# Performance work log

Hardware: AMD Instinct MI355X
Metric: run time of the kernel (lower is better)

## Reference

```python
import jax, jax.numpy as jnp
import numpy as np

N = 100000   # nodes
E = 1600000  # edges (avg degree 16)
D = 32       # feature dim

def setup_inputs() -> dict:
    key = jax.random.key(0)
    k1, k2, k3, k4 = jax.random.split(key, 4)
    feat = jax.random.normal(k1, (N, D), dtype=jnp.float32)
    e_feat = jax.random.normal(k2, (E, 1), dtype=jnp.float32)
    src = jax.random.randint(k3, (E,), 0, N)
    dst = jax.random.randint(k4, (E,), 0, N)
    return {"feat": feat, "e_feat": e_feat, "src": src, "dst": dst}

def reference(feat, e_feat, src, dst):
    n = feat.shape[0]
    ones = jnp.ones(src.shape[0], dtype=feat.dtype)
    # degrees computed on the full graph (before self-loop removal), as in DGL code
    out_deg = jax.ops.segment_sum(ones, src, num_segments=n)
    in_deg = jax.ops.segment_sum(ones, dst, num_segments=n)
    src_norm = jnp.power(jnp.clip(out_deg, 1.0, None), -0.5)[:, None]  # [N,1]
    dst_norm = jnp.power(jnp.clip(in_deg, 1.0, None), -0.5)[:, None]   # [N,1]
    # remove_self_loop: mask out self-loop edges in the aggregation only
    mask = (src != dst).astype(feat.dtype)[:, None]                    # [E,1]
    # u_mul_e: gather normalized src features, multiply by edge weight
    msg = (feat * src_norm)[src] * (e_feat * mask)                     # [E,D]
    agg = jax.ops.segment_sum(msg, dst, num_segments=n)                # [N,D]
    out = feat - agg * dst_norm
    return jnp.sum(jnp.abs(out), axis=1)                               # [N]
```

## Files before the change

kernel.cpp:

```cpp
#include <hip/hip_runtime.h>

#define D 32
#define RANGE 128
#define RMAX 800
#define JC 512
#define CHUNKMAX 3200
#define CAP 2304
#define SJC 256
#define SCHUNKMAX 6400
#define STRIDE 2560
#define SSTRIDE 2560
#define CPAD 16

__device__ __forceinline__ int scan512(int x, int* wp, int t) {
    int lane = t & 63, w = t >> 6;
    #pragma unroll
    for (int d = 1; d < 64; d <<= 1) {
        int y = __shfl_up(x, d, 64);
        if (lane >= d) x += y;
    }
    if (lane == 63) wp[w] = x;
    __syncthreads();
    int off = 0;
    #pragma unroll
    for (int i = 0; i < 7; i++) if (i < w) off += wp[i];
    return x + off;
}

__global__ __launch_bounds__(256) void zero_cur(int* __restrict__ p, int m) {
    int i = blockIdx.x * 256 + threadIdx.x;
    if (i < m) p[i] = 0;
}

__global__ __launch_bounds__(512) void fused_sort(
        const int* __restrict__ src, const int* __restrict__ dst,
        const float* __restrict__ ef,
        uint2* __restrict__ recsR, unsigned* __restrict__ srcsR,
        int* __restrict__ gcurD, int* __restrict__ gcurS,
        int E, int R, int chunk, int chunkS) {
    __shared__ __align__(16) char arena[32000];
    __shared__ int wp[8];
    int t = threadIdx.x;
    int* cnt = (int*)(arena + 25600);
    int* cur = (int*)(arena + 28800);

    if (blockIdx.x < JC) {
        int j = blockIdx.x;
        uint2* sd = (uint2*)arena;
        int e0 = j * chunk, e1 = min(E, e0 + chunk);
        for (int i = t; i < RMAX; i += 512) cnt[i] = 0;
        __syncthreads();
        for (int e = e0 + 2 * t; e < e1; e += 1024) {
            if (e + 1 < e1) {
                int2 d2 = *(const int2*)(dst + e);
                atomicAdd(&cnt[d2.x >> 7], 1);
                atomicAdd(&cnt[d2.y >> 7], 1);
            } else {
                atomicAdd(&cnt[dst[e] >> 7], 1);
            }
        }
        __syncthreads();
        int v0 = cnt[t];
        int incl0 = scan512(v0, wp, t);
        int tot0 = wp[0] + wp[1] + wp[2] + wp[3] + wp[4] + wp[5] + wp[6] + wp[7];
        __syncthreads();
        int i1 = t + 512;
        int v1 = (i1 < RMAX) ? cnt[i1] : 0;
        int incl1 = scan512(v1, wp, t);
        cur[t] = incl0 - v0;
        if (i1 < RMAX) cur[i1] = tot0 + incl1 - v1;
        __syncthreads();
        for (int e = e0 + t; e < e1; e += 512) {
            int s = src[e], d = dst[e];
            float w = (s == d) ? 0.0f : ef[e];
            int pos = atomicAdd(&cur[d >> 7], 1);
            sd[pos] = make_uint2((unsigned)s | ((unsigned)(d & (RANGE - 1)) << 17),
                                 __float_as_uint(w));
        }
        __syncthreads();
        for (int i = t; i < R; i += 512) {
            int c = cnt[i];
            if (c) {
                int g = atomicAdd(&gcurD[i * CPAD], c);
                int ls = cur[i] - c;
                uint2* dp = recsR + (size_t)i * STRIDE + g;
                for (int k = 0; k < c; k++) dp[k] = sd[ls + k];
            }
        }
    } else {
        int j = blockIdx.x - JC;
        unsigned* ids = (unsigned*)arena;
        int e0 = j * chunkS, e1 = min(E, e0 + chunkS);
        for (int i = t; i < RMAX; i += 512) cnt[i] = 0;
        __syncthreads();
        for (int e = e0 + 2 * t; e < e1; e += 1024) {
            if (e + 1 < e1) {
                int2 s2 = *(const int2*)(src + e);
                atomicAdd(&cnt[s2.x >> 7], 1);
                atomicAdd(&cnt[s2.y >> 7], 1);
            } else {
                atomicAdd(&cnt[src[e] >> 7], 1);
            }
        }
        __syncthreads();
        int v0 = cnt[t];
        int incl0 = scan512(v0, wp, t);
        int tot0 = wp[0] + wp[1] + wp[2] + wp[3] + wp[4] + wp[5] + wp[6] + wp[7];
        __syncthreads();
        int i1 = t + 512;
        int v1 = (i1 < RMAX) ? cnt[i1] : 0;
        int incl1 = scan512(v1, wp, t);
        cur[t] = incl0 - v0;
        if (i1 < RMAX) cur[i1] = tot0 + incl1 - v1;
        __syncthreads();
        for (int e = e0 + t; e < e1; e += 512) {
            unsigned s = (unsigned)src[e];
            int pos = atomicAdd(&cur[s >> 7], 1);
            ids[pos] = s;
        }
        __syncthreads();
        for (int i = t; i < R; i += 512) {
            int c = cnt[i];
            if (c) {
                int g = atomicAdd(&gcurS[i * CPAD], c);
                int ls = cur[i] - c;
                unsigned* dp = srcsR + (size_t)i * SSTRIDE + g;
                for (int k = 0; k < c; k++) dp[k] = ids[ls + k];
            }
        }
    }
}

__device__ __forceinline__ unsigned short f2bf(float x) {
    unsigned u = __float_as_uint(x);
    u += 0x7FFFu + ((u >> 16) & 1u);
    return (unsigned short)(u >> 16);
}

__global__ __launch_bounds__(512) void srcnorm_convert(
        const unsigned* __restrict__ srcsR, const int* __restrict__ gcurS,
        const float* __restrict__ feat, unsigned short* __restrict__ featb,
        int n, int R) {
    __shared__ int cnt[RANGE];
    int r = blockIdx.x, t = threadIdx.x;
    int base = r * RANGE, lim = min(n - base, RANGE);
    if (t < RANGE) cnt[t] = 0;
    __syncthreads();
    int total = gcurS[r * CPAD];
    const unsigned* p = srcsR + (size_t)r * SSTRIDE;
    for (int i = t; i < total; i += 512)
        atomicAdd(&cnt[p[i] - (unsigned)base], 1);
    __syncthreads();
    int total4 = lim * 8;
    for (int i = t; i < total4; i += 512) {
        int row = i >> 3;
        float sn = rsqrtf((float)max(cnt[row], 1));
        float4 f = ((const float4*)(feat + (size_t)(base + row) * D))[i & 7];
        ushort4 u;
        u.x = f2bf(f.x * sn); u.y = f2bf(f.y * sn);
        u.z = f2bf(f.z * sn); u.w = f2bf(f.w * sn);
        ((ushort4*)(featb + (size_t)(base + row) * D))[i & 7] = u;
    }
}

__global__ __launch_bounds__(512) void gather_kernel(
        const float* __restrict__ feat, const unsigned short* __restrict__ featb,
        const uint2* __restrict__ recsR, const int* __restrict__ gcurD,
        float* __restrict__ out, int n, int R) {
    __shared__ uint2 raw[CAP];
    __shared__ uint2 srec[CAP];
    __shared__ int indeg[RANGE];
    __shared__ int pre[RANGE + 1];
    __shared__ int wp[8];
    int r = blockIdx.x, t = threadIdx.x;
    int base = r * RANGE, lim = min(n - base, RANGE);
    int total = gcurD[r * CPAD];
    bool ovf = total > CAP;
    const uint2* reg = recsR + (size_t)r * STRIDE;
    if (t < RANGE) indeg[t] = 0;
    __syncthreads();
    if (!ovf) {
        for (int i = t; i < total; i += 512) {
            uint2 rec = reg[i];
            raw[i] = rec;
            atomicAdd(&indeg[rec.x >> 17], 1);
        }
    } else {
        for (int i = t; i < total; i += 512)
            atomicAdd(&indeg[reg[i].x >> 17], 1);
    }
    __syncthreads();
    int vv = (t < RANGE) ? indeg[t] : 0;
    int incl2 = scan512(vv, wp, t);
    if (t < RANGE) pre[t + 1] = incl2;
    if (t == 0) pre[0] = 0;
    __syncthreads();
    if (t < RANGE) indeg[t] = pre[t];
    __syncthreads();
    if (!ovf) {
        for (int i = t; i < total; i += 512) {
            uint2 rec = raw[i];
            int dl = rec.x >> 17;
            int pos = atomicAdd(&indeg[dl], 1);
            srec[pos] = make_uint2(rec.x & 0x1FFFFu, rec.y);
        }
    }
    __syncthreads();
    int node = t >> 2;
    int cch = t & 3;
    if (node >= lim) return;
    int p0i = pre[node];
    int cnt = pre[node + 1] - p0i;
    float a0 = 0.f, a1 = 0.f, a2 = 0.f, a3 = 0.f, a4 = 0.f, a5 = 0.f, a6 = 0.f, a7 = 0.f;
    if (!ovf) {
        const uint2* sp = srec + p0i;
        int i = 0;
        for (; i + 4 <= cnt; i += 4) {
            uint2 q0 = sp[i], q1 = sp[i + 1], q2 = sp[i + 2], q3 = sp[i + 3];
            uint4 b0 = ((const uint4*)(featb + (size_t)q0.x * D))[cch];
            uint4 b1 = ((const uint4*)(featb + (size_t)q1.x * D))[cch];
            uint4 b2 = ((const uint4*)(featb + (size_t)q2.x * D))[cch];
            uint4 b3 = ((const uint4*)(featb + (size_t)q3.x * D))[cch];
            float w0 = __uint_as_float(q0.y), w1 = __uint_as_float(q1.y);
            float w2 = __uint_as_float(q2.y), w3 = __uint_as_float(q3.y);
            a0 += __uint_as_float(b0.x << 16) * w0 + __uint_as_float(b1.x << 16) * w1
                + __uint_as_float(b2.x << 16) * w2 + __uint_as_float(b3.x << 16) * w3;
            a1 += __uint_as_float(b0.x & 0xFFFF0000u) * w0 + __uint_as_float(b1.x & 0xFFFF0000u) * w1
                + __uint_as_float(b2.x & 0xFFFF0000u) * w2 + __uint_as_float(b3.x & 0xFFFF0000u) * w3;
            a2 += __uint_as_float(b0.y << 16) * w0 + __uint_as_float(b1.y << 16) * w1
                + __uint_as_float(b2.y << 16) * w2 + __uint_as_float(b3.y << 16) * w3;
            a3 += __uint_as_float(b0.y & 0xFFFF0000u) * w0 + __uint_as_float(b1.y & 0xFFFF0000u) * w1
                + __uint_as_float(b2.y & 0xFFFF0000u) * w2 + __uint_as_float(b3.y & 0xFFFF0000u) * w3;
            a4 += __uint_as_float(b0.z << 16) * w0 + __uint_as_float(b1.z << 16) * w1
                + __uint_as_float(b2.z << 16) * w2 + __uint_as_float(b3.z << 16) * w3;
            a5 += __uint_as_float(b0.z & 0xFFFF0000u) * w0 + __uint_as_float(b1.z & 0xFFFF0000u) * w1
                + __uint_as_float(b2.z & 0xFFFF0000u) * w2 + __uint_as_float(b3.z & 0xFFFF0000u) * w3;
            a6 += __uint_as_float(b0.w << 16) * w0 + __uint_as_float(b1.w << 16) * w1
                + __uint_as_float(b2.w << 16) * w2 + __uint_as_float(b3.w << 16) * w3;
            a7 += __uint_as_float(b0.w & 0xFFFF0000u) * w0 + __uint_as_float(b1.w & 0xFFFF0000u) * w1
                + __uint_as_float(b2.w & 0xFFFF0000u) * w2 + __uint_as_float(b3.w & 0xFFFF0000u) * w3;
        }
        for (; i < cnt; i++) {
            uint2 q = sp[i];
            uint4 b = ((const uint4*)(featb + (size_t)q.x * D))[cch];
            float w = __uint_as_float(q.y);
            a0 += __uint_as_float(b.x << 16) * w;
            a1 += __uint_as_float(b.x & 0xFFFF0000u) * w;
            a2 += __uint_as_float(b.y << 16) * w;
            a3 += __uint_as_float(b.y & 0xFFFF0000u) * w;
            a4 += __uint_as_float(b.z << 16) * w;
            a5 += __uint_as_float(b.z & 0xFFFF0000u) * w;
            a6 += __uint_as_float(b.w << 16) * w;
            a7 += __uint_as_float(b.w & 0xFFFF0000u) * w;
        }
    } else {
        for (int k = 0; k < total; k++) {
            uint2 rec = reg[k];
            if ((int)(rec.x >> 17) == node) {
                uint4 b = ((const uint4*)(featb + (size_t)(rec.x & 0x1FFFFu) * D))[cch];
                float w = __uint_as_float(rec.y);
                a0 += __uint_as_float(b.x << 16) * w;
                a1 += __uint_as_float(b.x & 0xFFFF0000u) * w;
                a2 += __uint_as_float(b.y << 16) * w;
                a3 += __uint_as_float(b.y & 0xFFFF0000u) * w;
                a4 += __uint_as_float(b.z << 16) * w;
                a5 += __uint_as_float(b.z & 0xFFFF0000u) * w;
                a6 += __uint_as_float(b.w << 16) * w;
                a7 += __uint_as_float(b.w & 0xFFFF0000u) * w;
            }
        }
    }
    float dn = rsqrtf((float)max(cnt, 1));
    const float4* fr = (const float4*)(feat + (size_t)(base + node) * D);
    float4 fA = fr[cch * 2];
    float4 fB = fr[cch * 2 + 1];
    float v = fabsf(fA.x - a0 * dn) + fabsf(fA.y - a1 * dn) +
              fabsf(fA.z - a2 * dn) + fabsf(fA.w - a3 * dn) +
              fabsf(fB.x - a4 * dn) + fabsf(fB.y - a5 * dn) +
              fabsf(fB.z - a6 * dn) + fabsf(fB.w - a7 * dn);
    v += __shfl_xor(v, 1, 4);
    v += __shfl_xor(v, 2, 4);
    if (cch == 0) out[base + node] = v;
}

extern "C" void kernel_launch(void* const* d_in, const int* in_sizes, int n_in,
                              void* d_out, int out_size, void* d_ws, size_t ws_size,
                              hipStream_t stream) {
    const float* feat   = (const float*)d_in[0];
    const float* e_feat = (const float*)d_in[1];
    const int*   src    = (const int*)d_in[2];
    const int*   dst    = (const int*)d_in[3];
    const int E = in_sizes[2];
    const int n = in_sizes[0] / D;
    float* out = (float*)d_out;

    const int R = (n + RANGE - 1) / RANGE;
    const int chunk  = (((E + JC  - 1) / JC ) + 1) & ~1;
    const int chunkS = (((E + SJC - 1) / SJC) + 1) & ~1;

    char* p = (char*)d_ws;
    uint2* recsR    = (uint2*)p;    p += ((size_t)R * STRIDE * 8 + 15) & ~(size_t)15;
    unsigned* srcsR = (unsigned*)p; p += ((size_t)R * SSTRIDE * 4 + 15) & ~(size_t)15;
    int* gcurD      = (int*)p;      p += ((size_t)R * CPAD * 4 + 15) & ~(size_t)15;
    int* gcurS      = (int*)p;      p += ((size_t)R * CPAD * 4 + 15) & ~(size_t)15;
    unsigned short* featb = (unsigned short*)p;

    const int mcur = R * CPAD * 2;
    zero_cur<<<(mcur + 255) / 256, 256, 0, stream>>>(gcurD, mcur);

    fused_sort<<<JC + SJC, 512, 0, stream>>>(src, dst, e_feat, recsR, srcsR,
                                             gcurD, gcurS, E, R, chunk, chunkS);

    srcnorm_convert<<<R, 512, 0, stream>>>(srcsR, gcurS, feat, featb, n, R);

    gather_kernel<<<R, 512, 0, stream>>>(feat, featb, recsR, gcurD, out, n, R);
}
```

Before: 146.0 us.

## Coalesce bucket scatter, shrink src ids to bytes, use fp32 normalized features

The sort kernel now stores a per-record range tag in shared memory and writes bucketed records back in one flat loop, so consecutive threads store consecutive records. Previously each thread copied a whole bucket serially. Chunk sizes are now fixed (5000 dst edges, 9000 src edges per block) with a larger shared arena, and source ids are stored as 8-bit local offsets, which cuts write and read traffic. The normalized feature table is kept in fp32 instead of bf16, which doubles gather bytes but removes conversion work and rounding error. The src-degree histogram is also split into two shared copies to reduce atomic contention.

```diff
diff --git a/kernel.cpp b/kernel.cpp
--- a/kernel.cpp
+++ b/kernel.cpp
@@ -3,14 +3,15 @@
 #define D 32
 #define RANGE 128
 #define RMAX 800
-#define JC 512
-#define CHUNKMAX 3200
 #define CAP 2304
-#define SJC 256
-#define SCHUNKMAX 6400
 #define STRIDE 2560
 #define SSTRIDE 2560
 #define CPAD 16
+#define DCH 5000
+#define SCH 9000
+#define CNT_OFF 50000
+#define CUR_OFF 53200
+#define ARENA_SZ 56400
 
 __device__ __forceinline__ int scan512(int x, int* wp, int t) {
     int lane = t & 63, w = t >> 6;
@@ -35,19 +36,20 @@
 __global__ __launch_bounds__(512) void fused_sort(
         const int* __restrict__ src, const int* __restrict__ dst,
         const float* __restrict__ ef,
-        uint2* __restrict__ recsR, unsigned* __restrict__ srcsR,
+        uint2* __restrict__ recsR, unsigned char* __restrict__ srcsR,
         int* __restrict__ gcurD, int* __restrict__ gcurS,
-        int E, int R, int chunk, int chunkS) {
-    __shared__ __align__(16) char arena[32000];
+        int E, int DJC) {
+    __shared__ __align__(16) char arena[ARENA_SZ];
     __shared__ int wp[8];
     int t = threadIdx.x;
-    int* cnt = (int*)(arena + 25600);
-    int* cur = (int*)(arena + 28800);
-
-    if (blockIdx.x < JC) {
+    int* cnt = (int*)(arena + CNT_OFF);
+    int* cur = (int*)(arena + CUR_OFF);
+
+    if ((int)blockIdx.x < DJC) {
         int j = blockIdx.x;
         uint2* sd = (uint2*)arena;
-        int e0 = j * chunk, e1 = min(E, e0 + chunk);
+        unsigned short* rg16 = (unsigned short*)(arena + 40000);
+        int e0 = j * DCH, e1 = min(E, e0 + DCH), cntE = e1 - e0;
         for (int i = t; i < RMAX; i += 512) cnt[i] = 0;
         __syncthreads();
         for (int e = e0 + 2 * t; e < e1; e += 1024) {
@@ -73,24 +75,30 @@
         for (int e = e0 + t; e < e1; e += 512) {
             int s = src[e], d = dst[e];
             float w = (s == d) ? 0.0f : ef[e];
-            int pos = atomicAdd(&cur[d >> 7], 1);
-            sd[pos] = make_uint2((unsigned)s | ((unsigned)(d & (RANGE - 1)) << 17),
+            int rg = d >> 7;
+            int pos = atomicAdd(&cur[rg], 1);
+            sd[pos] = make_uint2((unsigned)s | ((unsigned)(d & 127) << 17),
                                  __float_as_uint(w));
-        }
-        __syncthreads();
-        for (int i = t; i < R; i += 512) {
+            rg16[pos] = (unsigned short)rg;
+        }
+        __syncthreads();
+        for (int i = t; i < RMAX; i += 512) {
             int c = cnt[i];
             if (c) {
                 int g = atomicAdd(&gcurD[i * CPAD], c);
-                int ls = cur[i] - c;
-                uint2* dp = recsR + (size_t)i * STRIDE + g;
-                for (int k = 0; k < c; k++) dp[k] = sd[ls + k];
-            }
+                cnt[i] = g - (cur[i] - c);
+            }
+        }
+        __syncthreads();
+        for (int i = t; i < cntE; i += 512) {
+            int rg = rg16[i];
+            recsR[(size_t)rg * STRIDE + cnt[rg] + i] = sd[i];
         }
     } else {
-        int j = blockIdx.x - JC;
-        unsigned* ids = (unsigned*)arena;
-        int e0 = j * chunkS, e1 = min(E, e0 + chunkS);
+        int j = blockIdx.x - DJC;
+        unsigned char* sid = (unsigned char*)arena;
+        unsigned short* rg16 = (unsigned short*)(arena + 9000);
+        int e0 = j * SCH, e1 = min(E, e0 + SCH), cntE = e1 - e0;
         for (int i = t; i < RMAX; i += 512) cnt[i] = 0;
         __syncthreads();
         for (int e = e0 + 2 * t; e < e1; e += 1024) {
@@ -114,57 +122,59 @@
         if (i1 < RMAX) cur[i1] = tot0 + incl1 - v1;
         __syncthreads();
         for (int e = e0 + t; e < e1; e += 512) {
-            unsigned s = (unsigned)src[e];
-            int pos = atomicAdd(&cur[s >> 7], 1);
-            ids[pos] = s;
-        }
-        __syncthreads();
-        for (int i = t; i < R; i += 512) {
+            int s = src[e];
+            int rg = s >> 7;
+            int pos = atomicAdd(&cur[rg], 1);
+            sid[pos] = (unsigned char)(s & 127);
+            rg16[pos] = (unsigned short)rg;
+        }
+        __syncthreads();
+        for (int i = t; i < RMAX; i += 512) {
             int c = cnt[i];
             if (c) {
                 int g = atomicAdd(&gcurS[i * CPAD], c);
-                int ls = cur[i] - c;
-                unsigned* dp = srcsR + (size_t)i * SSTRIDE + g;
-                for (int k = 0; k < c; k++) dp[k] = ids[ls + k];
-            }
-        }
-    }
-}
-
-__device__ __forceinline__ unsigned short f2bf(float x) {
-    unsigned u = __float_as_uint(x);
-    u += 0x7FFFu + ((u >> 16) & 1u);
-    return (unsigned short)(u >> 16);
+                cnt[i] = g - (cur[i] - c);
+            }
+        }
+        __syncthreads();
+        for (int i = t; i < cntE; i += 512) {
+            int rg = rg16[i];
+            srcsR[(size_t)rg * SSTRIDE + cnt[rg] + i] = sid[i];
+        }
+    }
 }
 
 __global__ __launch_bounds__(512) void srcnorm_convert(
-        const unsigned* __restrict__ srcsR, const int* __restrict__ gcurS,
-        const float* __restrict__ feat, unsigned short* __restrict__ featb,
+        const unsigned char* __restrict__ srcsR, const int* __restrict__ gcurS,
+        const float* __restrict__ feat, float* __restrict__ featn,
         int n, int R) {
+    __shared__ int h[2][RANGE];
     __shared__ int cnt[RANGE];
     int r = blockIdx.x, t = threadIdx.x;
     int base = r * RANGE, lim = min(n - base, RANGE);
-    if (t < RANGE) cnt[t] = 0;
+    if (t < 256) h[t >> 7][t & 127] = 0;
     __syncthreads();
     int total = gcurS[r * CPAD];
-    const unsigned* p = srcsR + (size_t)r * SSTRIDE;
+    const unsigned char* p = srcsR + (size_t)r * SSTRIDE;
+    int cp = (t >> 8) & 1;
     for (int i = t; i < total; i += 512)
-        atomicAdd(&cnt[p[i] - (unsigned)base], 1);
+        atomicAdd(&h[cp][p[i]], 1);
+    __syncthreads();
+    if (t < RANGE) cnt[t] = h[0][t] + h[1][t];
     __syncthreads();
     int total4 = lim * 8;
     for (int i = t; i < total4; i += 512) {
         int row = i >> 3;
         float sn = rsqrtf((float)max(cnt[row], 1));
         float4 f = ((const float4*)(feat + (size_t)(base + row) * D))[i & 7];
-        ushort4 u;
-        u.x = f2bf(f.x * sn); u.y = f2bf(f.y * sn);
-        u.z = f2bf(f.z * sn); u.w = f2bf(f.w * sn);
-        ((ushort4*)(featb + (size_t)(base + row) * D))[i & 7] = u;
+        float4 o;
+        o.x = f.x * sn; o.y = f.y * sn; o.z = f.z * sn; o.w = f.w * sn;
+        ((float4*)(featn + (size_t)(base + row) * D))[i & 7] = o;
     }
 }
 
 __global__ __launch_bounds__(512) void gather_kernel(
-        const float* __restrict__ feat, const unsigned short* __restrict__ featb,
+        const float* __restrict__ feat, const float* __restrict__ featn,
         const uint2* __restrict__ recsR, const int* __restrict__ gcurD,
         float* __restrict__ out, int n, int R) {
     __shared__ uint2 raw[CAP];
@@ -217,56 +227,42 @@
         int i = 0;
         for (; i + 4 <= cnt; i += 4) {
             uint2 q0 = sp[i], q1 = sp[i + 1], q2 = sp[i + 2], q3 = sp[i + 3];
-            uint4 b0 = ((const uint4*)(featb + (size_t)q0.x * D))[cch];
-            uint4 b1 = ((const uint4*)(featb + (size_t)q1.x * D))[cch];
-            uint4 b2 = ((const uint4*)(featb + (size_t)q2.x * D))[cch];
-            uint4 b3 = ((const uint4*)(featb + (size_t)q3.x * D))[cch];
+            const float4* f0 = (const float4*)(featn + (size_t)q0.x * D) + cch * 2;
+            const float4* f1 = (const float4*)(featn + (size_t)q1.x * D) + cch * 2;
+            const float4* f2 = (const float4*)(featn + (size_t)q2.x * D) + cch * 2;
+            const float4* f3 = (const float4*)(featn + (size_t)q3.x * D) + cch * 2;
+            float4 A0 = f0[0], B0 = f0[1];
+            float4 A1 = f1[0], B1 = f1[1];
+            float4 A2 = f2[0], B2 = f2[1];
+            float4 A3 = f3[0], B3 = f3[1];
             float w0 = __uint_as_float(q0.y), w1 = __uint_as_float(q1.y);
             float w2 = __uint_as_float(q2.y), w3 = __uint_as_float(q3.y);
-            a0 += __uint_as_float(b0.x << 16) * w0 + __uint_as_float(b1.x << 16) * w1
-                + __uint_as_float(b2.x << 16) * w2 + __uint_as_float(b3.x << 16) * w3;
-            a1 += __uint_as_float(b0.x & 0xFFFF0000u) * w0 + __uint_as_float(b1.x & 0xFFFF0000u) * w1
-                + __uint_as_float(b2.x & 0xFFFF0000u) * w2 + __uint_as_float(b3.x & 0xFFFF0000u) * w3;
-            a2 += __uint_as_float(b0.y << 16) * w0 + __uint_as_float(b1.y << 16) * w1
-                + __uint_as_float(b2.y << 16) * w2 + __uint_as_float(b3.y << 16) * w3;
-            a3 += __uint_as_float(b0.y & 0xFFFF0000u) * w0 + __uint_as_float(b1.y & 0xFFFF0000u) * w1
-                + __uint_as_float(b2.y & 0xFFFF0000u) * w2 + __uint_as_float(b3.y & 0xFFFF0000u) * w3;
-            a4 += __uint_as_float(b0.z << 16) * w0 + __uint_as_float(b1.z << 16) * w1
-                + __uint_as_float(b2.z << 16) * w2 + __uint_as_float(b3.z << 16) * w3;
-            a5 += __uint_as_float(b0.z & 0xFFFF0000u) * w0 + __uint_as_float(b1.z & 0xFFFF0000u) * w1
-                + __uint_as_float(b2.z & 0xFFFF0000u) * w2 + __uint_as_float(b3.z & 0xFFFF0000u) * w3;
-            a6 += __uint_as_float(b0.w << 16) * w0 + __uint_as_float(b1.w << 16) * w1
-                + __uint_as_float(b2.w << 16) * w2 + __uint_as_float(b3.w << 16) * w3;
-            a7 += __uint_as_float(b0.w & 0xFFFF0000u) * w0 + __uint_as_float(b1.w & 0xFFFF0000u) * w1
-                + __uint_as_float(b2.w & 0xFFFF0000u) * w2 + __uint_as_float(b3.w & 0xFFFF0000u) * w3;
+            a0 += A0.x * w0 + A1.x * w1 + A2.x * w2 + A3.x * w3;
+            a1 += A0.y * w0 + A1.y * w1 + A2.y * w2 + A3.y * w3;
+            a2 += A0.z * w0 + A1.z * w1 + A2.z * w2 + A3.z * w3;
+            a3 += A0.w * w0 + A1.w * w1 + A2.w * w2 + A3.w * w3;
+            a4 += B0.x * w0 + B1.x * w1 + B2.x * w2 + B3.x * w3;
+            a5 += B0.y * w0 + B1.y * w1 + B2.y * w2 + B3.y * w3;
+            a6 += B0.z * w0 + B1.z * w1 + B2.z * w2 + B3.z * w3;
+            a7 += B0.w * w0 + B1.w * w1 + B2.w * w2 + B3.w * w3;
         }
         for (; i < cnt; i++) {
             uint2 q = sp[i];
-            uint4 b = ((const uint4*)(featb + (size_t)q.x * D))[cch];
+            const float4* f = (const float4*)(featn + (size_t)q.x * D) + cch * 2;
+            float4 A = f[0], B = f[1];
             float w = __uint_as_float(q.y);
-            a0 += __uint_as_float(b.x << 16) * w;
-            a1 += __uint_as_float(b.x & 0xFFFF0000u) * w;
-            a2 += __uint_as_float(b.y << 16) * w;
-            a3 += __uint_as_float(b.y & 0xFFFF0000u) * w;
-            a4 += __uint_as_float(b.z << 16) * w;
-            a5 += __uint_as_float(b.z & 0xFFFF0000u) * w;
-            a6 += __uint_as_float(b.w << 16) * w;
-            a7 += __uint_as_float(b.w & 0xFFFF0000u) * w;
+            a0 += A.x * w; a1 += A.y * w; a2 += A.z * w; a3 += A.w * w;
+            a4 += B.x * w; a5 += B.y * w; a6 += B.z * w; a7 += B.w * w;
         }
     } else {
         for (int k = 0; k < total; k++) {
             uint2 rec = reg[k];
             if ((int)(rec.x >> 17) == node) {
-                uint4 b = ((const uint4*)(featb + (size_t)(rec.x & 0x1FFFFu) * D))[cch];
+                const float4* f = (const float4*)(featn + (size_t)(rec.x & 0x1FFFFu) * D) + cch * 2;
+                float4 A = f[0], B = f[1];
                 float w = __uint_as_float(rec.y);
-                a0 += __uint_as_float(b.x << 16) * w;
-                a1 += __uint_as_float(b.x & 0xFFFF0000u) * w;
-                a2 += __uint_as_float(b.y << 16) * w;
-                a3 += __uint_as_float(b.y & 0xFFFF0000u) * w;
-                a4 += __uint_as_float(b.z << 16) * w;
-                a5 += __uint_as_float(b.z & 0xFFFF0000u) * w;
-                a6 += __uint_as_float(b.w << 16) * w;
-                a7 += __uint_as_float(b.w & 0xFFFF0000u) * w;
+                a0 += A.x * w; a1 += A.y * w; a2 += A.z * w; a3 += A.w * w;
+                a4 += B.x * w; a5 += B.y * w; a6 += B.z * w; a7 += B.w * w;
             }
         }
     }
@@ -294,24 +290,24 @@
     const int n = in_sizes[0] / D;
     float* out = (float*)d_out;
 
-    const int R = (n + RANGE - 1) / RANGE;
-    const int chunk  = (((E + JC  - 1) / JC ) + 1) & ~1;
-    const int chunkS = (((E + SJC - 1) / SJC) + 1) & ~1;
+    const int R   = (n + RANGE - 1) / RANGE;
+    const int DJC = (E + DCH - 1) / DCH;
+    const int SJC = (E + SCH - 1) / SCH;
 
     char* p = (char*)d_ws;
-    uint2* recsR    = (uint2*)p;    p += ((size_t)R * STRIDE * 8 + 15) & ~(size_t)15;
-    unsigned* srcsR = (unsigned*)p; p += ((size_t)R * SSTRIDE * 4 + 15) & ~(size_t)15;
-    int* gcurD      = (int*)p;      p += ((size_t)R * CPAD * 4 + 15) & ~(size_t)15;
-    int* gcurS      = (int*)p;      p += ((size_t)R * CPAD * 4 + 15) & ~(size_t)15;
-    unsigned short* featb = (unsigned short*)p;
+    uint2* recsR        = (uint2*)p;         p += ((size_t)R * STRIDE * 8 + 15) & ~(size_t)15;
+    unsigned char* srcsR = (unsigned char*)p; p += ((size_t)R * SSTRIDE + 15) & ~(size_t)15;
+    int* gcurD          = (int*)p;           p += ((size_t)2 * R * CPAD * 4 + 15) & ~(size_t)15;
+    int* gcurS          = gcurD + (size_t)R * CPAD;
+    float* featn        = (float*)p;
 
     const int mcur = R * CPAD * 2;
     zero_cur<<<(mcur + 255) / 256, 256, 0, stream>>>(gcurD, mcur);
 
-    fused_sort<<<JC + SJC, 512, 0, stream>>>(src, dst, e_feat, recsR, srcsR,
-                                             gcurD, gcurS, E, R, chunk, chunkS);
-
-    srcnorm_convert<<<R, 512, 0, stream>>>(srcsR, gcurS, feat, featb, n, R);
-
-    gather_kernel<<<R, 512, 0, stream>>>(feat, featb, recsR, gcurD, out, n, R);
-}
+    fused_sort<<<DJC + SJC, 512, 0, stream>>>(src, dst, e_feat, recsR, srcsR,
+                                              gcurD, gcurS, E, DJC);
+
+    srcnorm_convert<<<R, 512, 0, stream>>>(srcsR, gcurS, feat, featn, n, R);
+
+    gather_kernel<<<R, 512, 0, stream>>>(feat, featn, recsR, gcurD, out, n, R);
+}
```

Result: faster. 140.6 us (-3.7%).
